# Kernel optimization log

Hardware: AMD Instinct MI355X
Metric: run time of the kernel (lower is better)

## Reference

```python
import jax, jax.numpy as jnp
import numpy as np

B, T, D = 4, 8192, 1024
BLOCKS, TOPK, MACRO, SLOTS = 64, 16, 4, 64
RMS_EPS = 1.1920929e-07  # torch.finfo(float32).eps, F.rms_norm default


def setup_inputs() -> dict:
    key = jax.random.key(0)
    ks = jax.random.split(key, 7)
    return {
        "prev_hidden": jax.random.normal(ks[0], (B, T, D), jnp.float32),
        "prev_nll": jax.random.uniform(ks[1], (B, T), jnp.float32),
        "query": jax.random.normal(ks[2], (SLOTS, D), jnp.float32) * 0.02,
        "W_sum": jax.random.normal(ks[3], (D, 2 * D), jnp.float32) / np.sqrt(2 * D),
        "W_k": jax.random.normal(ks[4], (D, D), jnp.float32) / np.sqrt(D),
        "W_v": jax.random.normal(ks[5], (D, D), jnp.float32) / np.sqrt(D),
        "W_o": jax.random.normal(ks[6], (D, D), jnp.float32) / np.sqrt(D),
    }


def _rms_norm(x):
    return x * jax.lax.rsqrt(jnp.mean(x * x, axis=-1, keepdims=True) + RMS_EPS)


def _zscore(x):
    m = x.mean(axis=1, keepdims=True)
    s = jnp.maximum(x.std(axis=1, keepdims=True), 1e-6)  # unbiased=False
    return (x - m) / s


def reference(prev_hidden, prev_nll, query, W_sum, W_k, W_v, W_o):
    b, t, d = prev_hidden.shape
    # --- micro segments: equal blocks (t divisible by BLOCKS -> linspace edges exact)
    L = t // BLOCKS
    seg = prev_hidden.reshape(b, BLOCKS, L, d)
    seg_mean = seg.mean(axis=2)          # [B, BLOCKS, D]
    seg_last = seg[:, :, -1, :]          # [B, BLOCKS, D]
    hid_score = jnp.linalg.norm(seg_mean, axis=-1)            # [B, BLOCKS]
    sur_score = prev_nll.reshape(b, BLOCKS, L).mean(axis=-1)  # [B, BLOCKS]
    scores = _zscore(hid_score) + _zscore(sur_score)          # utility_source='both'
    idx = jnp.sort(jax.lax.top_k(scores, TOPK)[1], axis=-1)   # [B, TOPK]
    gmean = jnp.take_along_axis(seg_mean, idx[:, :, None], axis=1)
    glast = jnp.take_along_axis(seg_last, idx[:, :, None], axis=1)
    micro = jnp.concatenate([gmean, glast], axis=-1)          # [B, TOPK, 2D]
    # --- hierarchical: macro segments + global
    Lm = t // MACRO
    mseg = prev_hidden.reshape(b, MACRO, Lm, d)
    macro = jnp.concatenate([mseg.mean(axis=2), mseg[:, :, -1, :]], axis=-1)
    glob = jnp.concatenate([prev_hidden.mean(axis=1), prev_hidden[:, -1, :]], axis=-1)[:, None, :]
    feats = jnp.concatenate([micro, macro, glob], axis=1)     # [B, S=21, 2D]
    summaries = _rms_norm(jnp.einsum('bsf,df->bsd', feats, W_sum))
    # --- cross-attention of learned prefix queries over sources
    keys = jnp.einsum('bsd,ed->bse', summaries, W_k)
    vals = jnp.einsum('bsd,ed->bse', summaries, W_v)
    logits = jnp.einsum('qd,bsd->bqs', query, keys) / jnp.sqrt(jnp.float32(d))
    attn = jax.nn.softmax(logits.astype(jnp.float32), axis=-1).astype(summaries.dtype)
    prefix = jnp.einsum('bqs,bse->bqe', attn, vals)
    return jnp.einsum('bqe,oe->bqo', prefix, W_o)
```

## Files before the change

### kernel.cpp

```cpp
#include <hip/hip_runtime.h>
#include <stdint.h>
#include <stddef.h>

#define B_ 4
#define T_ 8192
#define D_ 1024
#define NBLK 64
#define SEGL 128
#define TOPK_ 16
#define NS 21
#define MPAD 96
#define RMS_EPS_ 1.1920929e-07f
#define PART 98304

typedef float f32x4 __attribute__((ext_vector_type(4)));
typedef __bf16 bf16x8 __attribute__((ext_vector_type(8)));
typedef unsigned short us8 __attribute__((ext_vector_type(8)));

__device__ __forceinline__ unsigned short f2bf(float f) {
    union { float f; unsigned int u; } v; v.f = f;
    unsigned int r = v.u + 0x7FFFu + ((v.u >> 16) & 1u);
    return (unsigned short)(r >> 16);
}
__device__ __forceinline__ float4 ld4(const float* p) { return *(const float4*)p; }

__global__ __launch_bounds__(512) void seg_stats(
        const float* __restrict__ ph, const float* __restrict__ nll,
        float* __restrict__ seg_mean, float* __restrict__ hid, float* __restrict__ sur) {
    int g = blockIdx.x; int b = g >> 6; int blk = g & 63;
    int tid = threadIdx.x; int half = tid >> 8; int c = tid & 255;
    const float* base = ph + ((size_t)b * T_ + blk * SEGL + half * 64) * D_ + 4 * c;
    float ax = 0.f, ay = 0.f, az = 0.f, aw = 0.f;
    #pragma unroll 8
    for (int r = 0; r < 64; r++) {
        float4 v = ld4(base + (size_t)r * D_);
        ax += v.x; ay += v.y; az += v.z; aw += v.w;
    }
    __shared__ float4 tmp[256];
    __shared__ float red[256];
    __shared__ float nl[128];
    if (tid < 128) nl[tid] = nll[b * T_ + blk * SEGL + tid];
    if (half) { float4 t; t.x = ax; t.y = ay; t.z = az; t.w = aw; tmp[c] = t; }
    __syncthreads();
    if (!half) {
        float4 t2 = tmp[c];
        float mx = (ax + t2.x) * (1.f/128.f), my = (ay + t2.y) * (1.f/128.f);
        float mz = (az + t2.z) * (1.f/128.f), mw = (aw + t2.w) * (1.f/128.f);
        float4 m; m.x = mx; m.y = my; m.z = mz; m.w = mw;
        *(float4*)(seg_mean + (size_t)g * D_ + 4 * c) = m;
        red[c] = mx*mx + my*my + mz*mz + mw*mw;
    }
    __syncthreads();
    for (int s2 = 128; s2 > 0; s2 >>= 1) { if (tid < s2) red[tid] += red[tid + s2]; __syncthreads(); }
    for (int s2 = 64;  s2 > 0; s2 >>= 1) { if (tid < s2) nl[tid]  += nl[tid + s2];  __syncthreads(); }
    if (tid == 0) { hid[g] = sqrtf(red[0]); sur[g] = nl[0] * (1.f/128.f); }
}

__global__ __launch_bounds__(256) void feats_build(
        const float* __restrict__ ph, const float* __restrict__ seg_mean,
        const float* __restrict__ hid, const float* __restrict__ sur,
        unsigned short* __restrict__ feats) {
    int r = blockIdx.x; int t = threadIdx.x;
    unsigned short* row0 = feats + (size_t)r * 2048 + 4 * t;
    unsigned short* row1 = row0 + 1024;
    if (r >= B_ * NS) {
        ushort4 z4; z4.x = z4.y = z4.z = z4.w = 0;
        *(ushort4*)row0 = z4; *(ushort4*)row1 = z4;
        return;
    }
    int b = r / NS, s = r % NS;
    __shared__ float sc[64];
    __shared__ int sidx[16];
    if (t < 64) {
        float h = hid[b * NBLK + t];
        float ss0 = sur[b * NBLK + t];
        float mh = h; for (int o = 32; o; o >>= 1) mh += __shfl_xor(mh, o); mh *= (1.f/64.f);
        float dh = h - mh; float vh = dh * dh;
        for (int o = 32; o; o >>= 1) vh += __shfl_xor(vh, o); vh *= (1.f/64.f);
        float sh = fmaxf(sqrtf(vh), 1e-6f);
        float ms = ss0; for (int o = 32; o; o >>= 1) ms += __shfl_xor(ms, o); ms *= (1.f/64.f);
        float ds = ss0 - ms; float vs = ds * ds;
        for (int o = 32; o; o >>= 1) vs += __shfl_xor(vs, o); vs *= (1.f/64.f);
        float ssd = fmaxf(sqrtf(vs), 1e-6f);
        sc[t] = dh / sh + ds / ssd;
    }
    __syncthreads();
    if (t < 64) {
        float z = sc[t];
        int rank = 0;
        for (int j = 0; j < 64; j++) {
            float oj = sc[j];
            rank += (oj > z) || (oj == z && j < t);
        }
        bool sel = rank < TOPK_;
        unsigned long long mask = __ballot(sel);
        int pos = __popcll(mask & ((1ull << t) - 1ull));
        if (sel) sidx[pos] = t;
    }
    __syncthreads();

    float mx = 0, my = 0, mz = 0, mw = 0;
    int lastrow;
    if (s < 16) {
        int blk = sidx[s];
        float4 v = ld4(seg_mean + (size_t)(b * NBLK + blk) * D_ + 4 * t);
        mx = v.x; my = v.y; mz = v.z; mw = v.w;
        lastrow = blk * SEGL + SEGL - 1;
    } else if (s < 20) {
        int m = s - 16;
        for (int j = 0; j < 16; j++) {
            float4 v = ld4(seg_mean + (size_t)(b * NBLK + m * 16 + j) * D_ + 4 * t);
            mx += v.x; my += v.y; mz += v.z; mw += v.w;
        }
        mx *= (1.f/16.f); my *= (1.f/16.f); mz *= (1.f/16.f); mw *= (1.f/16.f);
        lastrow = m * 2048 + 2047;
    } else {
        for (int j = 0; j < 64; j++) {
            float4 v = ld4(seg_mean + (size_t)(b * NBLK + j) * D_ + 4 * t);
            mx += v.x; my += v.y; mz += v.z; mw += v.w;
        }
        mx *= (1.f/64.f); my *= (1.f/64.f); mz *= (1.f/64.f); mw *= (1.f/64.f);
        lastrow = T_ - 1;
    }
    float4 lv = ld4(ph + ((size_t)b * T_ + lastrow) * D_ + 4 * t);
    ushort4 hm; hm.x = f2bf(mx); hm.y = f2bf(my); hm.z = f2bf(mz); hm.w = f2bf(mw);
    ushort4 hl; hl.x = f2bf(lv.x); hl.y = f2bf(lv.y); hl.z = f2bf(lv.z); hl.w = f2bf(lv.w);
    *(ushort4*)row0 = hm;
    *(ushort4*)row1 = hl;
}

template<int K, int AMODE>
__global__ __launch_bounds__(512) void gemm_lds(
        const void* __restrict__ Av,
        const float* __restrict__ B0, const float* __restrict__ B1,
        float* __restrict__ C0, float* __restrict__ C1) {
    const float* Bw = blockIdx.z ? B1 : B0;
    float* Cp       = blockIdx.z ? C1 : C0;
    int n0 = blockIdx.x * 64;
    int kc = blockIdx.y;
    Cp += (size_t)kc * PART;
    int tid = threadIdx.x, wave = tid >> 6, lane = tid & 63;
    int quad = lane >> 4, l16 = lane & 15;

    __shared__ unsigned short Bs[64 * 264];
    __shared__ unsigned short As[96 * 264];

    #pragma unroll
    for (int i = 0; i < 4; i++) {
        int id = tid + 512 * i;
        int r = id >> 5, c = id & 31;
        const float* src = Bw + (size_t)(n0 + r) * K + kc * 256 + c * 8;
        float4 v0 = ld4(src), v1 = ld4(src + 4);
        us8 h;
        h[0] = f2bf(v0.x); h[1] = f2bf(v0.y); h[2] = f2bf(v0.z); h[3] = f2bf(v0.w);
        h[4] = f2bf(v1.x); h[5] = f2bf(v1.y); h[6] = f2bf(v1.z); h[7] = f2bf(v1.w);
        *(us8*)&Bs[r * 264 + c * 8] = h;
    }
    #pragma unroll
    for (int i = 0; i < 6; i++) {
        int id = tid + 512 * i;
        int r = id >> 5, c = id & 31;
        if (AMODE == 0) {
            const unsigned short* A = (const unsigned short*)Av;
            *(us8*)&As[r * 264 + c * 8] =
                *(const us8*)(A + (size_t)r * K + kc * 256 + c * 8);
        } else {
            const float* A = (const float*)Av;
            const float* s0 = A + (size_t)r * 1024 + kc * 256 + c * 8;
            float4 a0 = ld4(s0), a1 = ld4(s0 + 4);
            #pragma unroll
            for (int p = 1; p < 4; p++) {
                float4 b0 = ld4(s0 + p * PART), b1 = ld4(s0 + p * PART + 4);
                a0.x += b0.x; a0.y += b0.y; a0.z += b0.z; a0.w += b0.w;
                a1.x += b1.x; a1.y += b1.y; a1.z += b1.z; a1.w += b1.w;
            }
            us8 h;
            h[0] = f2bf(a0.x); h[1] = f2bf(a0.y); h[2] = f2bf(a0.z); h[3] = f2bf(a0.w);
            h[4] = f2bf(a1.x); h[5] = f2bf(a1.y); h[6] = f2bf(a1.z); h[7] = f2bf(a1.w);
            *(us8*)&As[r * 264 + c * 8] = h;
        }
    }
    __syncthreads();

    int strip = wave >> 1, kh = wave & 1;
    f32x4 acc[6];
    #pragma unroll
    for (int i = 0; i < 6; i++) acc[i] = (f32x4){0.f, 0.f, 0.f, 0.f};
    const unsigned short* bbase = &Bs[(strip * 16 + l16) * 264 + kh * 128 + quad * 8];
    const unsigned short* abase = &As[l16 * 264 + kh * 128 + quad * 8];
    #pragma unroll
    for (int kk = 0; kk < 128; kk += 32) {
        bf16x8 bfr = __builtin_bit_cast(bf16x8, *(const us8*)(bbase + kk));
        #pragma unroll
        for (int mi = 0; mi < 6; mi++) {
            bf16x8 af = __builtin_bit_cast(bf16x8, *(const us8*)(abase + mi * 16 * 264 + kk));
            acc[mi] = __builtin_amdgcn_mfma_f32_16x16x32_bf16(af, bfr, acc[mi], 0, 0, 0);
        }
    }
    __syncthreads();

    float* scr = (float*)As;
    if (kh == 1) {
        #pragma unroll
        for (int mi = 0; mi < 6; mi++)
            #pragma unroll
            for (int r = 0; r < 4; r++)
                scr[((strip * 6 + mi) * 16 + quad * 4 + r) * 16 + l16] = acc[mi][r];
    }
    __syncthreads();
    if (kh == 0) {
        #pragma unroll
        for (int mi = 0; mi < 6; mi++)
            #pragma unroll
            for (int r = 0; r < 4; r++) {
                float v = acc[mi][r] + scr[((strip * 6 + mi) * 16 + quad * 4 + r) * 16 + l16];
                Cp[(size_t)(mi * 16 + quad * 4 + r) * 1024 + n0 + strip * 16 + l16] = v;
            }
    }
}

__global__ __launch_bounds__(256) void rmsnorm8(
        const float* __restrict__ pp, unsigned short* __restrict__ y) {
    int r = blockIdx.x; int t = threadIdx.x;
    float4 v = (float4){0.f, 0.f, 0.f, 0.f};
    #pragma unroll
    for (int c = 0; c < 8; c++) {
        float4 u = ld4(pp + (size_t)c * PART + (size_t)r * D_ + 4 * t);
        v.x += u.x; v.y += u.y; v.z += u.z; v.w += u.w;
    }
    __shared__ float red[256];
    red[t] = v.x*v.x + v.y*v.y + v.z*v.z + v.w*v.w;
    __syncthreads();
    for (int s2 = 128; s2 > 0; s2 >>= 1) { if (t < s2) red[t] += red[t + s2]; __syncthreads(); }
    float scale = rsqrtf(red[0] * (1.f/1024.f) + RMS_EPS_);
    ushort4 h;
    h.x = f2bf(v.x * scale); h.y = f2bf(v.y * scale);
    h.z = f2bf(v.z * scale); h.w = f2bf(v.w * scale);
    *(ushort4*)(y + (size_t)r * D_ + 4 * t) = h;
}

__global__ __launch_bounds__(256) void attn_out(
        const float* __restrict__ query, const float* __restrict__ keys_p,
        const float* __restrict__ valsO_p, float* __restrict__ out) {
    int g = blockIdx.x; int b = g >> 6; int q = g & 63;
    int tid = threadIdx.x, wave = tid >> 6, lane = tid & 63;
    __shared__ float attnw[24];
    const float* qrow = query + (size_t)q * D_ + lane * 16;
    float4 qv0 = ld4(qrow), qv1 = ld4(qrow + 4), qv2 = ld4(qrow + 8), qv3 = ld4(qrow + 12);
    for (int s = wave; s < NS; s += 4) {
        const float* krow = keys_p + (size_t)(b * NS + s) * D_ + lane * 16;
        float4 k0 = (float4){0,0,0,0}, k1 = k0, k2 = k0, k3 = k0;
        #pragma unroll
        for (int c = 0; c < 4; c++) {
            const float* kp = krow + (size_t)c * PART;
            float4 u0 = ld4(kp), u1 = ld4(kp + 4), u2 = ld4(kp + 8), u3 = ld4(kp + 12);
            k0.x += u0.x; k0.y += u0.y; k0.z += u0.z; k0.w += u0.w;
            k1.x += u1.x; k1.y += u1.y; k1.z += u1.z; k1.w += u1.w;
            k2.x += u2.x; k2.y += u2.y; k2.z += u2.z; k2.w += u2.w;
            k3.x += u3.x; k3.y += u3.y; k3.z += u3.z; k3.w += u3.w;
        }
        float a = qv0.x*k0.x + qv0.y*k0.y + qv0.z*k0.z + qv0.w*k0.w
                + qv1.x*k1.x + qv1.y*k1.y + qv1.z*k1.z + qv1.w*k1.w
                + qv2.x*k2.x + qv2.y*k2.y + qv2.z*k2.z + qv2.w*k2.w
                + qv3.x*k3.x + qv3.y*k3.y + qv3.z*k3.z + qv3.w*k3.w;
        for (int o = 32; o; o >>= 1) a += __shfl_xor(a, o);
        if (lane == 0) attnw[s] = a * 0.03125f;
    }
    __syncthreads();
    if (tid == 0) {
        float mx = -1e30f;
        for (int s = 0; s < NS; s++) mx = fmaxf(mx, attnw[s]);
        float sum = 0.f;
        for (int s = 0; s < NS; s++) { float e = expf(attnw[s] - mx); attnw[s] = e; sum += e; }
        float inv = 1.f / sum;
        for (int s = 0; s < NS; s++) attnw[s] *= inv;
    }
    __syncthreads();
    float ax = 0, ay = 0, az = 0, aw = 0;
    #pragma unroll
    for (int s = 0; s < NS; s++) {
        float w = attnw[s];
        float4 v = (float4){0,0,0,0};
        #pragma unroll
        for (int c = 0; c < 4; c++) {
            float4 u = ld4(valsO_p + (size_t)c * PART + (size_t)(b * NS + s) * D_ + 4 * tid);
            v.x += u.x; v.y += u.y; v.z += u.z; v.w += u.w;
        }
        ax += w * v.x; ay += w * v.y; az += w * v.z; aw += w * v.w;
    }
    float4 o4; o4.x = ax; o4.y = ay; o4.z = az; o4.w = aw;
    *(float4*)(out + (size_t)g * D_ + 4 * tid) = o4;
}

extern "C" void kernel_launch(void* const* d_in, const int* in_sizes, int n_in,
                              void* d_out, int out_size, void* d_ws, size_t ws_size,
                              hipStream_t stream) {
    (void)in_sizes; (void)n_in; (void)out_size; (void)ws_size;
    const float* ph    = (const float*)d_in[0];
    const float* nll   = (const float*)d_in[1];
    const float* query = (const float*)d_in[2];
    const float* W_sum = (const float*)d_in[3];
    const float* W_k   = (const float*)d_in[4];
    const float* W_v   = (const float*)d_in[5];
    const float* W_o   = (const float*)d_in[6];
    float* out = (float*)d_out;

    char* ws = (char*)d_ws;
    float*          seg_mean = (float*)(ws + 0);
    float*          hid      = (float*)(ws + 1048576);
    float*          sur      = (float*)(ws + 1049600);
    unsigned short* feats    = (unsigned short*)(ws + 1050624);
    float*          presum_p = (float*)(ws + 1443840);
    unsigned short* summ_b   = (unsigned short*)(ws + 4589568);
    float*          keys_p   = (float*)(ws + 4786176);
    float*          vals_p   = (float*)(ws + 6359040);
    float*          valsO_p  = (float*)(ws + 7931904);

    seg_stats<<<B_ * NBLK, 512, 0, stream>>>(ph, nll, seg_mean, hid, sur);
    feats_build<<<MPAD, 256, 0, stream>>>(ph, seg_mean, hid, sur, feats);
    gemm_lds<2048, 0><<<dim3(16, 8, 1), 512, 0, stream>>>(
        feats, W_sum, nullptr, presum_p, nullptr);
    rmsnorm8<<<MPAD, 256, 0, stream>>>(presum_p, summ_b);
    gemm_lds<1024, 0><<<dim3(16, 4, 2), 512, 0, stream>>>(
        summ_b, W_k, W_v, keys_p, vals_p);
    gemm_lds<1024, 1><<<dim3(16, 4, 1), 512, 0, stream>>>(
        vals_p, W_o, nullptr, valsO_p, nullptr);
    attn_out<<<B_ * NBLK, 256, 0, stream>>>(query, keys_p, valsO_p, out);
}
```

Baseline: 256.4 us.

## Precompute W_o·W_v product and fuse tail stages into cooperative megakernel

Folds the value and output projections into one weight X = W_o·W_v, computed in bf16 MFMA by extra blocks of the segment-statistics kernel so it runs alongside the bandwidth-bound hidden-state reduction. The remaining small stages (feature build, W_sum GEMM, RMS norm, key/value GEMMs, attention) are merged into a single 128-block cooperative kernel separated by grid syncs. This removes several kernel launches and one dependent GEMM stage. In exchange the weight product is recomputed every call, adds bf16 rounding of X, and grid-wide syncs replace the launch boundaries.

Result: slower. 373.2 us (+45.6%).

```diff
diff --git a/kernel.cpp b/kernel.cpp
--- a/kernel.cpp
+++ b/kernel.cpp
@@ -1,6 +1,9 @@
 #include <hip/hip_runtime.h>
+#include <hip/hip_cooperative_groups.h>
 #include <stdint.h>
 #include <stddef.h>
+
+namespace cg = cooperative_groups;
 
 #define B_ 4
 #define T_ 8192
@@ -24,168 +27,151 @@
 }
 __device__ __forceinline__ float4 ld4(const float* p) { return *(const float4*)p; }
 
-__global__ __launch_bounds__(512) void seg_stats(
+__global__ __launch_bounds__(512) void seg_wc(
         const float* __restrict__ ph, const float* __restrict__ nll,
-        float* __restrict__ seg_mean, float* __restrict__ hid, float* __restrict__ sur) {
-    int g = blockIdx.x; int b = g >> 6; int blk = g & 63;
-    int tid = threadIdx.x; int half = tid >> 8; int c = tid & 255;
-    const float* base = ph + ((size_t)b * T_ + blk * SEGL + half * 64) * D_ + 4 * c;
-    float ax = 0.f, ay = 0.f, az = 0.f, aw = 0.f;
-    #pragma unroll 8
-    for (int r = 0; r < 64; r++) {
-        float4 v = ld4(base + (size_t)r * D_);
-        ax += v.x; ay += v.y; az += v.z; aw += v.w;
-    }
+        const float* __restrict__ W_o, const float* __restrict__ W_v,
+        float* __restrict__ seg_mean, float* __restrict__ hid, float* __restrict__ sur,
+        unsigned short* __restrict__ X) {
     __shared__ float4 tmp[256];
     __shared__ float red[256];
     __shared__ float nl[128];
-    if (tid < 128) nl[tid] = nll[b * T_ + blk * SEGL + tid];
-    if (half) { float4 t; t.x = ax; t.y = ay; t.z = az; t.w = aw; tmp[c] = t; }
-    __syncthreads();
-    if (!half) {
-        float4 t2 = tmp[c];
-        float mx = (ax + t2.x) * (1.f/128.f), my = (ay + t2.y) * (1.f/128.f);
-        float mz = (az + t2.z) * (1.f/128.f), mw = (aw + t2.w) * (1.f/128.f);
-        float4 m; m.x = mx; m.y = my; m.z = mz; m.w = mw;
-        *(float4*)(seg_mean + (size_t)g * D_ + 4 * c) = m;
-        red[c] = mx*mx + my*my + mz*mz + mw*mw;
-    }
-    __syncthreads();
-    for (int s2 = 128; s2 > 0; s2 >>= 1) { if (tid < s2) red[tid] += red[tid + s2]; __syncthreads(); }
-    for (int s2 = 64;  s2 > 0; s2 >>= 1) { if (tid < s2) nl[tid]  += nl[tid + s2];  __syncthreads(); }
-    if (tid == 0) { hid[g] = sqrtf(red[0]); sur[g] = nl[0] * (1.f/128.f); }
+    __shared__ unsigned short As2[128 * 136];
+    __shared__ unsigned short Bt[128 * 136];
+
+    int bx = blockIdx.x;
+    int tid = threadIdx.x;
+
+    if (bx < 256) {
+        int b = bx >> 6; int blk = bx & 63;
+        int half = tid >> 8; int c = tid & 255;
+        const float* base = ph + ((size_t)b * T_ + blk * SEGL + half * 64) * D_ + 4 * c;
+        float ax = 0.f, ay = 0.f, az = 0.f, aw = 0.f;
+        #pragma unroll 8
+        for (int r = 0; r < 64; r++) {
+            float4 v = ld4(base + (size_t)r * D_);
+            ax += v.x; ay += v.y; az += v.z; aw += v.w;
+        }
+        if (tid < 128) nl[tid] = nll[b * T_ + blk * SEGL + tid];
+        if (half) { float4 t; t.x = ax; t.y = ay; t.z = az; t.w = aw; tmp[c] = t; }
+        __syncthreads();
+        if (!half) {
+            float4 t2 = tmp[c];
+            float mx = (ax + t2.x) * (1.f/128.f), my = (ay + t2.y) * (1.f/128.f);
+            float mz = (az + t2.z) * (1.f/128.f), mw = (aw + t2.w) * (1.f/128.f);
+            float4 m; m.x = mx; m.y = my; m.z = mz; m.w = mw;
+            *(float4*)(seg_mean + (size_t)bx * D_ + 4 * c) = m;
+            red[c] = mx*mx + my*my + mz*mz + mw*mw;
+        }
+        __syncthreads();
+        for (int s2 = 128; s2 > 0; s2 >>= 1) { if (tid < s2) red[tid] += red[tid + s2]; __syncthreads(); }
+        for (int s2 = 64;  s2 > 0; s2 >>= 1) { if (tid < s2) nl[tid]  += nl[tid + s2];  __syncthreads(); }
+        if (tid == 0) { hid[bx] = sqrtf(red[0]); sur[bx] = nl[0] * (1.f/128.f); }
+        return;
+    }
+
+    int w = bx - 256;
+    int m0 = (w >> 3) * 128;
+    int n0 = (w & 7) * 128;
+    int wave = tid >> 6, lane = tid & 63;
+    int quad = lane >> 4, l16 = lane & 15;
+    int mi2 = wave >> 2, ni2 = wave & 3;
+
+    f32x4 acc[4][2];
+    #pragma unroll
+    for (int a = 0; a < 4; a++)
+        #pragma unroll
+        for (int b2 = 0; b2 < 2; b2++) acc[a][b2] = (f32x4){0.f,0.f,0.f,0.f};
+
+    for (int kc = 0; kc < 8; kc++) {
+        #pragma unroll
+        for (int i = 0; i < 4; i++) {
+            int id = tid + 512 * i;
+            int r = id >> 4, c = id & 15;
+            const float* src = W_o + (size_t)(m0 + r) * 1024 + kc * 128 + c * 8;
+            float4 v0 = ld4(src), v1 = ld4(src + 4);
+            us8 h;
+            h[0]=f2bf(v0.x); h[1]=f2bf(v0.y); h[2]=f2bf(v0.z); h[3]=f2bf(v0.w);
+            h[4]=f2bf(v1.x); h[5]=f2bf(v1.y); h[6]=f2bf(v1.z); h[7]=f2bf(v1.w);
+            *(us8*)&As2[r * 136 + c * 8] = h;
+        }
+        #pragma unroll
+        for (int i = 0; i < 4; i++) {
+            int id = tid + 512 * i;
+            int e = id >> 4, dc = id & 15;
+            const float* src = W_v + (size_t)(kc * 128 + e) * 1024 + n0 + dc * 8;
+            float4 v0 = ld4(src), v1 = ld4(src + 4);
+            float vv[8] = {v0.x,v0.y,v0.z,v0.w,v1.x,v1.y,v1.z,v1.w};
+            #pragma unroll
+            for (int j = 0; j < 8; j++)
+                Bt[(dc * 8 + j) * 136 + e] = f2bf(vv[j]);
+        }
+        __syncthreads();
+        #pragma unroll
+        for (int kk = 0; kk < 128; kk += 32) {
+            #pragma unroll
+            for (int nt = 0; nt < 2; nt++) {
+                bf16x8 bfr = __builtin_bit_cast(bf16x8,
+                    *(const us8*)&Bt[(ni2 * 32 + nt * 16 + l16) * 136 + kk + quad * 8]);
+                #pragma unroll
+                for (int mt = 0; mt < 4; mt++) {
+                    bf16x8 af = __builtin_bit_cast(bf16x8,
+                        *(const us8*)&As2[(mi2 * 64 + mt * 16 + l16) * 136 + kk + quad * 8]);
+                    acc[mt][nt] = __builtin_amdgcn_mfma_f32_16x16x32_bf16(af, bfr, acc[mt][nt], 0, 0, 0);
+                }
+            }
+        }
+        __syncthreads();
+    }
+    #pragma unroll
+    for (int mt = 0; mt < 4; mt++)
+        #pragma unroll
+        for (int nt = 0; nt < 2; nt++)
+            #pragma unroll
+            for (int r = 0; r < 4; r++) {
+                int row = m0 + mi2 * 64 + mt * 16 + quad * 4 + r;
+                int col = n0 + ni2 * 32 + nt * 16 + l16;
+                X[(size_t)row * 1024 + col] = f2bf(acc[mt][nt][r]);
+            }
 }
 
-__global__ __launch_bounds__(256) void feats_build(
-        const float* __restrict__ ph, const float* __restrict__ seg_mean,
-        const float* __restrict__ hid, const float* __restrict__ sur,
-        unsigned short* __restrict__ feats) {
-    int r = blockIdx.x; int t = threadIdx.x;
-    unsigned short* row0 = feats + (size_t)r * 2048 + 4 * t;
-    unsigned short* row1 = row0 + 1024;
-    if (r >= B_ * NS) {
-        ushort4 z4; z4.x = z4.y = z4.z = z4.w = 0;
-        *(ushort4*)row0 = z4; *(ushort4*)row1 = z4;
-        return;
-    }
-    int b = r / NS, s = r % NS;
-    __shared__ float sc[64];
-    __shared__ int sidx[16];
-    if (t < 64) {
-        float h = hid[b * NBLK + t];
-        float ss0 = sur[b * NBLK + t];
-        float mh = h; for (int o = 32; o; o >>= 1) mh += __shfl_xor(mh, o); mh *= (1.f/64.f);
-        float dh = h - mh; float vh = dh * dh;
-        for (int o = 32; o; o >>= 1) vh += __shfl_xor(vh, o); vh *= (1.f/64.f);
-        float sh = fmaxf(sqrtf(vh), 1e-6f);
-        float ms = ss0; for (int o = 32; o; o >>= 1) ms += __shfl_xor(ms, o); ms *= (1.f/64.f);
-        float ds = ss0 - ms; float vs = ds * ds;
-        for (int o = 32; o; o >>= 1) vs += __shfl_xor(vs, o); vs *= (1.f/64.f);
-        float ssd = fmaxf(sqrtf(vs), 1e-6f);
-        sc[t] = dh / sh + ds / ssd;
-    }
-    __syncthreads();
-    if (t < 64) {
-        float z = sc[t];
-        int rank = 0;
-        for (int j = 0; j < 64; j++) {
-            float oj = sc[j];
-            rank += (oj > z) || (oj == z && j < t);
-        }
-        bool sel = rank < TOPK_;
-        unsigned long long mask = __ballot(sel);
-        int pos = __popcll(mask & ((1ull << t) - 1ull));
-        if (sel) sidx[pos] = t;
-    }
-    __syncthreads();
-
-    float mx = 0, my = 0, mz = 0, mw = 0;
-    int lastrow;
-    if (s < 16) {
-        int blk = sidx[s];
-        float4 v = ld4(seg_mean + (size_t)(b * NBLK + blk) * D_ + 4 * t);
-        mx = v.x; my = v.y; mz = v.z; mw = v.w;
-        lastrow = blk * SEGL + SEGL - 1;
-    } else if (s < 20) {
-        int m = s - 16;
-        for (int j = 0; j < 16; j++) {
-            float4 v = ld4(seg_mean + (size_t)(b * NBLK + m * 16 + j) * D_ + 4 * t);
-            mx += v.x; my += v.y; mz += v.z; mw += v.w;
-        }
-        mx *= (1.f/16.f); my *= (1.f/16.f); mz *= (1.f/16.f); mw *= (1.f/16.f);
-        lastrow = m * 2048 + 2047;
-    } else {
-        for (int j = 0; j < 64; j++) {
-            float4 v = ld4(seg_mean + (size_t)(b * NBLK + j) * D_ + 4 * t);
-            mx += v.x; my += v.y; mz += v.z; mw += v.w;
-        }
-        mx *= (1.f/64.f); my *= (1.f/64.f); mz *= (1.f/64.f); mw *= (1.f/64.f);
-        lastrow = T_ - 1;
-    }
-    float4 lv = ld4(ph + ((size_t)b * T_ + lastrow) * D_ + 4 * t);
-    ushort4 hm; hm.x = f2bf(mx); hm.y = f2bf(my); hm.z = f2bf(mz); hm.w = f2bf(mw);
-    ushort4 hl; hl.x = f2bf(lv.x); hl.y = f2bf(lv.y); hl.z = f2bf(lv.z); hl.w = f2bf(lv.w);
-    *(ushort4*)row0 = hm;
-    *(ushort4*)row1 = hl;
-}
-
-template<int K, int AMODE>
-__global__ __launch_bounds__(512) void gemm_lds(
-        const void* __restrict__ Av,
-        const float* __restrict__ B0, const float* __restrict__ B1,
-        float* __restrict__ C0, float* __restrict__ C1) {
-    const float* Bw = blockIdx.z ? B1 : B0;
-    float* Cp       = blockIdx.z ? C1 : C0;
-    int n0 = blockIdx.x * 64;
-    int kc = blockIdx.y;
+__device__ __forceinline__ void gemm_chunk(
+        const unsigned short* __restrict__ Abf,
+        const float* __restrict__ Bf32, const unsigned short* __restrict__ Bbf,
+        int K, int n0, int kc, float* __restrict__ Cp,
+        unsigned short* Bs, unsigned short* As, int tid) {
     Cp += (size_t)kc * PART;
-    int tid = threadIdx.x, wave = tid >> 6, lane = tid & 63;
+    int wave = tid >> 6, lane = tid & 63;
     int quad = lane >> 4, l16 = lane & 15;
-
-    __shared__ unsigned short Bs[64 * 264];
-    __shared__ unsigned short As[96 * 264];
 
     #pragma unroll
     for (int i = 0; i < 4; i++) {
         int id = tid + 512 * i;
         int r = id >> 5, c = id & 31;
-        const float* src = Bw + (size_t)(n0 + r) * K + kc * 256 + c * 8;
-        float4 v0 = ld4(src), v1 = ld4(src + 4);
-        us8 h;
-        h[0] = f2bf(v0.x); h[1] = f2bf(v0.y); h[2] = f2bf(v0.z); h[3] = f2bf(v0.w);
-        h[4] = f2bf(v1.x); h[5] = f2bf(v1.y); h[6] = f2bf(v1.z); h[7] = f2bf(v1.w);
-        *(us8*)&Bs[r * 264 + c * 8] = h;
+        if (Bf32) {
+            const float* src = Bf32 + (size_t)(n0 + r) * K + kc * 256 + c * 8;
+            float4 v0 = ld4(src), v1 = ld4(src + 4);
+            us8 h;
+            h[0]=f2bf(v0.x); h[1]=f2bf(v0.y); h[2]=f2bf(v0.z); h[3]=f2bf(v0.w);
+            h[4]=f2bf(v1.x); h[5]=f2bf(v1.y); h[6]=f2bf(v1.z); h[7]=f2bf(v1.w);
+            *(us8*)&Bs[r * 264 + c * 8] = h;
+        } else {
+            *(us8*)&Bs[r * 264 + c * 8] =
+                *(const us8*)(Bbf + (size_t)(n0 + r) * K + kc * 256 + c * 8);
+        }
     }
     #pragma unroll
     for (int i = 0; i < 6; i++) {
         int id = tid + 512 * i;
         int r = id >> 5, c = id & 31;
-        if (AMODE == 0) {
-            const unsigned short* A = (const unsigned short*)Av;
-            *(us8*)&As[r * 264 + c * 8] =
-                *(const us8*)(A + (size_t)r * K + kc * 256 + c * 8);
-        } else {
-            const float* A = (const float*)Av;
-            const float* s0 = A + (size_t)r * 1024 + kc * 256 + c * 8;
-            float4 a0 = ld4(s0), a1 = ld4(s0 + 4);
-            #pragma unroll
-            for (int p = 1; p < 4; p++) {
-                float4 b0 = ld4(s0 + p * PART), b1 = ld4(s0 + p * PART + 4);
-                a0.x += b0.x; a0.y += b0.y; a0.z += b0.z; a0.w += b0.w;
-                a1.x += b1.x; a1.y += b1.y; a1.z += b1.z; a1.w += b1.w;
-            }
-            us8 h;
-            h[0] = f2bf(a0.x); h[1] = f2bf(a0.y); h[2] = f2bf(a0.z); h[3] = f2bf(a0.w);
-            h[4] = f2bf(a1.x); h[5] = f2bf(a1.y); h[6] = f2bf(a1.z); h[7] = f2bf(a1.w);
-            *(us8*)&As[r * 264 + c * 8] = h;
-        }
+        *(us8*)&As[r * 264 + c * 8] =
+            *(const us8*)(Abf + (size_t)r * K + kc * 256 + c * 8);
     }
     __syncthreads();
 
     int strip = wave >> 1, kh = wave & 1;
     f32x4 acc[6];
     #pragma unroll
-    for (int i = 0; i < 6; i++) acc[i] = (f32x4){0.f, 0.f, 0.f, 0.f};
+    for (int i = 0; i < 6; i++) acc[i] = (f32x4){0.f,0.f,0.f,0.f};
     const unsigned short* bbase = &Bs[(strip * 16 + l16) * 264 + kh * 128 + quad * 8];
     const unsigned short* abase = &As[l16 * 264 + kh * 128 + quad * 8];
     #pragma unroll
@@ -198,7 +184,6 @@
         }
     }
     __syncthreads();
-
     float* scr = (float*)As;
     if (kh == 1) {
         #pragma unroll
@@ -219,77 +204,180 @@
     }
 }
 
-__global__ __launch_bounds__(256) void rmsnorm8(
-        const float* __restrict__ pp, unsigned short* __restrict__ y) {
-    int r = blockIdx.x; int t = threadIdx.x;
-    float4 v = (float4){0.f, 0.f, 0.f, 0.f};
-    #pragma unroll
-    for (int c = 0; c < 8; c++) {
-        float4 u = ld4(pp + (size_t)c * PART + (size_t)r * D_ + 4 * t);
-        v.x += u.x; v.y += u.y; v.z += u.z; v.w += u.w;
-    }
-    __shared__ float red[256];
-    red[t] = v.x*v.x + v.y*v.y + v.z*v.z + v.w*v.w;
-    __syncthreads();
-    for (int s2 = 128; s2 > 0; s2 >>= 1) { if (t < s2) red[t] += red[t + s2]; __syncthreads(); }
-    float scale = rsqrtf(red[0] * (1.f/1024.f) + RMS_EPS_);
-    ushort4 h;
-    h.x = f2bf(v.x * scale); h.y = f2bf(v.y * scale);
-    h.z = f2bf(v.z * scale); h.w = f2bf(v.w * scale);
-    *(ushort4*)(y + (size_t)r * D_ + 4 * t) = h;
-}
-
-__global__ __launch_bounds__(256) void attn_out(
-        const float* __restrict__ query, const float* __restrict__ keys_p,
-        const float* __restrict__ valsO_p, float* __restrict__ out) {
-    int g = blockIdx.x; int b = g >> 6; int q = g & 63;
-    int tid = threadIdx.x, wave = tid >> 6, lane = tid & 63;
-    __shared__ float attnw[24];
-    const float* qrow = query + (size_t)q * D_ + lane * 16;
-    float4 qv0 = ld4(qrow), qv1 = ld4(qrow + 4), qv2 = ld4(qrow + 8), qv3 = ld4(qrow + 12);
-    for (int s = wave; s < NS; s += 4) {
-        const float* krow = keys_p + (size_t)(b * NS + s) * D_ + lane * 16;
-        float4 k0 = (float4){0,0,0,0}, k1 = k0, k2 = k0, k3 = k0;
-        #pragma unroll
-        for (int c = 0; c < 4; c++) {
-            const float* kp = krow + (size_t)c * PART;
-            float4 u0 = ld4(kp), u1 = ld4(kp + 4), u2 = ld4(kp + 8), u3 = ld4(kp + 12);
-            k0.x += u0.x; k0.y += u0.y; k0.z += u0.z; k0.w += u0.w;
-            k1.x += u1.x; k1.y += u1.y; k1.z += u1.z; k1.w += u1.w;
-            k2.x += u2.x; k2.y += u2.y; k2.z += u2.z; k2.w += u2.w;
-            k3.x += u3.x; k3.y += u3.y; k3.z += u3.z; k3.w += u3.w;
-        }
-        float a = qv0.x*k0.x + qv0.y*k0.y + qv0.z*k0.z + qv0.w*k0.w
-                + qv1.x*k1.x + qv1.y*k1.y + qv1.z*k1.z + qv1.w*k1.w
-                + qv2.x*k2.x + qv2.y*k2.y + qv2.z*k2.z + qv2.w*k2.w
-                + qv3.x*k3.x + qv3.y*k3.y + qv3.z*k3.z + qv3.w*k3.w;
-        for (int o = 32; o; o >>= 1) a += __shfl_xor(a, o);
-        if (lane == 0) attnw[s] = a * 0.03125f;
-    }
-    __syncthreads();
-    if (tid == 0) {
-        float mx = -1e30f;
-        for (int s = 0; s < NS; s++) mx = fmaxf(mx, attnw[s]);
-        float sum = 0.f;
-        for (int s = 0; s < NS; s++) { float e = expf(attnw[s] - mx); attnw[s] = e; sum += e; }
-        float inv = 1.f / sum;
-        for (int s = 0; s < NS; s++) attnw[s] *= inv;
-    }
-    __syncthreads();
-    float ax = 0, ay = 0, az = 0, aw = 0;
-    #pragma unroll
-    for (int s = 0; s < NS; s++) {
-        float w = attnw[s];
-        float4 v = (float4){0,0,0,0};
-        #pragma unroll
-        for (int c = 0; c < 4; c++) {
-            float4 u = ld4(valsO_p + (size_t)c * PART + (size_t)(b * NS + s) * D_ + 4 * tid);
-            v.x += u.x; v.y += u.y; v.z += u.z; v.w += u.w;
-        }
-        ax += w * v.x; ay += w * v.y; az += w * v.z; aw += w * v.w;
-    }
-    float4 o4; o4.x = ax; o4.y = ay; o4.z = az; o4.w = aw;
-    *(float4*)(out + (size_t)g * D_ + 4 * tid) = o4;
+__global__ __launch_bounds__(512) void megatail(
+        const float* __restrict__ ph, const float* __restrict__ seg_mean,
+        const float* __restrict__ hid, const float* __restrict__ sur,
+        unsigned short* __restrict__ feats, const float* __restrict__ W_sum,
+        float* __restrict__ presum_p, unsigned short* __restrict__ summ_b,
+        const float* __restrict__ W_k, const unsigned short* __restrict__ X,
+        float* __restrict__ keys_p, float* __restrict__ valsO_p,
+        const float* __restrict__ query, float* __restrict__ out) {
+    __shared__ unsigned short Bs[64 * 264];
+    __shared__ unsigned short As[96 * 264];
+    cg::grid_group grid = cg::this_grid();
+    int bx = blockIdx.x;
+    int tid = threadIdx.x;
+
+    if (bx < MPAD) {
+        int r = bx;
+        float* sc = (float*)Bs;
+        int* sidx = (int*)(Bs + 256);
+        int b = r / NS, s = r % NS;
+        if (tid < 64) {
+            float h = hid[b * NBLK + tid];
+            float ss0 = sur[b * NBLK + tid];
+            float mh = h; for (int o = 32; o; o >>= 1) mh += __shfl_xor(mh, o); mh *= (1.f/64.f);
+            float dh = h - mh; float vh = dh * dh;
+            for (int o = 32; o; o >>= 1) vh += __shfl_xor(vh, o); vh *= (1.f/64.f);
+            float sh = fmaxf(sqrtf(vh), 1e-6f);
+            float ms = ss0; for (int o = 32; o; o >>= 1) ms += __shfl_xor(ms, o); ms *= (1.f/64.f);
+            float ds = ss0 - ms; float vs = ds * ds;
+            for (int o = 32; o; o >>= 1) vs += __shfl_xor(vs, o); vs *= (1.f/64.f);
+            float ssd = fmaxf(sqrtf(vs), 1e-6f);
+            sc[tid] = dh / sh + ds / ssd;
+        }
+        __syncthreads();
+        if (tid < 64) {
+            float z = sc[tid];
+            int rank = 0;
+            for (int j = 0; j < 64; j++) {
+                float oj = sc[j];
+                rank += (oj > z) || (oj == z && j < tid);
+            }
+            bool sel = rank < TOPK_;
+            unsigned long long mask = __ballot(sel);
+            int pos = __popcll(mask & ((1ull << tid) - 1ull));
+            if (sel) sidx[pos] = tid;
+        }
+        __syncthreads();
+        if (tid < 256) {
+            int t = tid;
+            unsigned short* row0 = feats + (size_t)r * 2048 + 4 * t;
+            unsigned short* row1 = row0 + 1024;
+            if (b >= B_) {
+                ushort4 z4; z4.x = z4.y = z4.z = z4.w = 0;
+                *(ushort4*)row0 = z4; *(ushort4*)row1 = z4;
+            } else {
+                float mx = 0, my = 0, mz = 0, mw = 0;
+                int lastrow;
+                if (s < 16) {
+                    int blk = sidx[s];
+                    float4 v = ld4(seg_mean + (size_t)(b * NBLK + blk) * D_ + 4 * t);
+                    mx = v.x; my = v.y; mz = v.z; mw = v.w;
+                    lastrow = blk * SEGL + SEGL - 1;
+                } else if (s < 20) {
+                    int m = s - 16;
+                    for (int j = 0; j < 16; j++) {
+                        float4 v = ld4(seg_mean + (size_t)(b * NBLK + m * 16 + j) * D_ + 4 * t);
+                        mx += v.x; my += v.y; mz += v.z; mw += v.w;
+                    }
+                    mx *= (1.f/16.f); my *= (1.f/16.f); mz *= (1.f/16.f); mw *= (1.f/16.f);
+                    lastrow = m * 2048 + 2047;
+                } else {
+                    for (int j = 0; j < 64; j++) {
+                        float4 v = ld4(seg_mean + (size_t)(b * NBLK + j) * D_ + 4 * t);
+                        mx += v.x; my += v.y; mz += v.z; mw += v.w;
+                    }
+                    mx *= (1.f/64.f); my *= (1.f/64.f); mz *= (1.f/64.f); mw *= (1.f/64.f);
+                    lastrow = T_ - 1;
+                }
+                float4 lv = ld4(ph + ((size_t)b * T_ + lastrow) * D_ + 4 * t);
+                ushort4 hm; hm.x = f2bf(mx); hm.y = f2bf(my); hm.z = f2bf(mz); hm.w = f2bf(mw);
+                ushort4 hl; hl.x = f2bf(lv.x); hl.y = f2bf(lv.y); hl.z = f2bf(lv.z); hl.w = f2bf(lv.w);
+                *(ushort4*)row0 = hm;
+                *(ushort4*)row1 = hl;
+            }
+        }
+    }
+    grid.sync();
+
+    gemm_chunk(feats, W_sum, nullptr, 2048, (bx & 15) * 64, bx >> 4,
+               presum_p, Bs, As, tid);
+    grid.sync();
+
+    if (bx < MPAD) {
+        float* red = (float*)Bs;
+        float4 v = (float4){0.f,0.f,0.f,0.f};
+        if (tid < 256) {
+            #pragma unroll
+            for (int c = 0; c < 8; c++) {
+                float4 u = ld4(presum_p + (size_t)c * PART + (size_t)bx * D_ + 4 * tid);
+                v.x += u.x; v.y += u.y; v.z += u.z; v.w += u.w;
+            }
+        }
+        red[tid] = (tid < 256) ? (v.x*v.x + v.y*v.y + v.z*v.z + v.w*v.w) : 0.f;
+        __syncthreads();
+        for (int s2 = 256; s2 > 0; s2 >>= 1) { if (tid < s2) red[tid] += red[tid + s2]; __syncthreads(); }
+        float scale = rsqrtf(red[0] * (1.f/1024.f) + RMS_EPS_);
+        if (tid < 256) {
+            ushort4 h;
+            h.x = f2bf(v.x * scale); h.y = f2bf(v.y * scale);
+            h.z = f2bf(v.z * scale); h.w = f2bf(v.w * scale);
+            *(ushort4*)(summ_b + (size_t)bx * D_ + 4 * tid) = h;
+        }
+    }
+    grid.sync();
+
+    {
+        int z = bx >> 6, rem = bx & 63;
+        int n = rem & 15, kc = rem >> 4;
+        if (z == 0) gemm_chunk(summ_b, W_k, nullptr, 1024, n * 64, kc, keys_p,  Bs, As, tid);
+        else        gemm_chunk(summ_b, nullptr, X,   1024, n * 64, kc, valsO_p, Bs, As, tid);
+    }
+    grid.sync();
+
+    {
+        float* attnw = (float*)Bs;
+        int sub = tid >> 8, tid2 = tid & 255;
+        int g = bx + 128 * sub;
+        int b = g >> 6, q = g & 63;
+        int wave4 = tid2 >> 6, lane = tid & 63;
+        const float* qrow = query + (size_t)q * D_ + lane * 16;
+        float4 qv0 = ld4(qrow), qv1 = ld4(qrow + 4), qv2 = ld4(qrow + 8), qv3 = ld4(qrow + 12);
+        for (int s = wave4; s < NS; s += 4) {
+            const float* krow = keys_p + (size_t)(b * NS + s) * D_ + lane * 16;
+            float4 k0 = (float4){0,0,0,0}, k1 = k0, k2 = k0, k3 = k0;
+            #pragma unroll
+            for (int c = 0; c < 4; c++) {
+                const float* kp = krow + (size_t)c * PART;
+                float4 u0 = ld4(kp), u1 = ld4(kp + 4), u2 = ld4(kp + 8), u3 = ld4(kp + 12);
+                k0.x += u0.x; k0.y += u0.y; k0.z += u0.z; k0.w += u0.w;
+                k1.x += u1.x; k1.y += u1.y; k1.z += u1.z; k1.w += u1.w;
+                k2.x += u2.x; k2.y += u2.y; k2.z += u2.z; k2.w += u2.w;
+                k3.x += u3.x; k3.y += u3.y; k3.z += u3.z; k3.w += u3.w;
+            }
+            float a = qv0.x*k0.x + qv0.y*k0.y + qv0.z*k0.z + qv0.w*k0.w
+                    + qv1.x*k1.x + qv1.y*k1.y + qv1.z*k1.z + qv1.w*k1.w
+                    + qv2.x*k2.x + qv2.y*k2.y + qv2.z*k2.z + qv2.w*k2.w
+                    + qv3.x*k3.x + qv3.y*k3.y + qv3.z*k3.z + qv3.w*k3.w;
+            for (int o = 32; o; o >>= 1) a += __shfl_xor(a, o);
+            if ((tid & 63) == 0) attnw[sub * 24 + s] = a * 0.03125f;
+        }
+        __syncthreads();
+        if (tid2 == 0) {
+            float mx = -1e30f;
+            for (int s = 0; s < NS; s++) mx = fmaxf(mx, attnw[sub * 24 + s]);
+            float sum = 0.f;
+            for (int s = 0; s < NS; s++) { float e = expf(attnw[sub * 24 + s] - mx); attnw[sub * 24 + s] = e; sum += e; }
+            float inv = 1.f / sum;
+            for (int s = 0; s < NS; s++) attnw[sub * 24 + s] *= inv;
+        }
+        __syncthreads();
+        float ax = 0, ay = 0, az = 0, aw = 0;
+        #pragma unroll
+        for (int s = 0; s < NS; s++) {
+            float wgt = attnw[sub * 24 + s];
+            float4 v = (float4){0,0,0,0};
+            #pragma unroll
+            for (int c = 0; c < 4; c++) {
+                float4 u = ld4(valsO_p + (size_t)c * PART + (size_t)(b * NS + s) * D_ + 4 * tid2);
+                v.x += u.x; v.y += u.y; v.z += u.z; v.w += u.w;
+            }
+            ax += wgt * v.x; ay += wgt * v.y; az += wgt * v.z; aw += wgt * v.w;
+        }
+        float4 o4; o4.x = ax; o4.y = ay; o4.z = az; o4.w = aw;
+        *(float4*)(out + (size_t)g * D_ + 4 * tid2) = o4;
+    }
 }
 
 extern "C" void kernel_launch(void* const* d_in, const int* in_sizes, int n_in,
@@ -313,17 +401,17 @@
     float*          presum_p = (float*)(ws + 1443840);
     unsigned short* summ_b   = (unsigned short*)(ws + 4589568);
     float*          keys_p   = (float*)(ws + 4786176);
-    float*          vals_p   = (float*)(ws + 6359040);
-    float*          valsO_p  = (float*)(ws + 7931904);
-
-    seg_stats<<<B_ * NBLK, 512, 0, stream>>>(ph, nll, seg_mean, hid, sur);
-    feats_build<<<MPAD, 256, 0, stream>>>(ph, seg_mean, hid, sur, feats);
-    gemm_lds<2048, 0><<<dim3(16, 8, 1), 512, 0, stream>>>(
-        feats, W_sum, nullptr, presum_p, nullptr);
-    rmsnorm8<<<MPAD, 256, 0, stream>>>(presum_p, summ_b);
-    gemm_lds<1024, 0><<<dim3(16, 4, 2), 512, 0, stream>>>(
-        summ_b, W_k, W_v, keys_p, vals_p);
-    gemm_lds<1024, 1><<<dim3(16, 4, 1), 512, 0, stream>>>(
-        vals_p, W_o, nullptr, valsO_p, nullptr);
-    attn_out<<<B_ * NBLK, 256, 0, stream>>>(query, keys_p, valsO_p, out);
+    float*          valsO_p  = (float*)(ws + 6359040);
+    unsigned short* X        = (unsigned short*)(ws + 7931904);
+
+    seg_wc<<<320, 512, 0, stream>>>(ph, nll, W_o, W_v, seg_mean, hid, sur, X);
+
+    void* args[] = {
+        (void*)&ph, (void*)&seg_mean, (void*)&hid, (void*)&sur,
+        (void*)&feats, (void*)&W_sum, (void*)&presum_p, (void*)&summ_b,
+        (void*)&W_k, (void*)&X, (void*)&keys_p, (void*)&valsO_p,
+        (void*)&query, (void*)&out
+    };
+    hipLaunchCooperativeKernel((const void*)megatail, dim3(128), dim3(512),
+                               args, 0, stream);
 }
```
